# Optimization experiments

Measured on AMD Instinct MI355X. Metric: run time of the kernel, lower is better.

The kernel has to match this reference:

```python
import jax, jax.numpy as jnp
import numpy as np

EPS = 1e-6

def setup_inputs() -> dict:
    key = jax.random.key(0)
    k1, k2, k3 = jax.random.split(key, 3)
    B, N, F, OUT = 16, 1024, 64, 128
    x = jax.random.normal(k1, (B, N, F), dtype=jnp.float32)
    A = jax.random.uniform(k2, (B, N, N), dtype=jnp.float32)
    kernel = jax.random.normal(k3, (3 * F, OUT), dtype=jnp.float32) * 0.05
    bias = jnp.zeros((OUT,), dtype=jnp.float32)
    return {"x": x, "A": A, "kernel": kernel, "bias": bias}


def reference(x, A, kernel, bias):
    # x: [B,N,F], A: [B,N,N]
    n = A.shape[-1]
    eye = jnp.eye(n, dtype=A.dtype)
    Az = A * (1.0 - eye)          # zero out diagonal (A -= diag(diag_part(A)))
    A_hat = Az + eye              # add self-loops
    deg = A_hat.sum(axis=2)       # [B,N]
    inv_asym = 1.0 / (EPS + deg)                 # D^{-1}
    s = 1.0 / (EPS + jnp.sqrt(deg))              # D^{-1/2}
    # Three message-passing variants; apply diagonal scalings as broadcasts
    o1 = jnp.matmul(Az, x)                                   # A x
    o2 = inv_asym[:, :, None] * jnp.matmul(A_hat, x)         # D^{-1} A_hat x
    o3 = s[:, :, None] * jnp.matmul(A_hat, s[:, :, None] * x)  # D^{-1/2} A_hat D^{-1/2} x
    out = jnp.concatenate([o1, o2, o3], axis=-1)             # [B,N,3F]
    out = jnp.matmul(out, kernel) + bias                     # [B,N,OUT]
    return jax.nn.relu(out)
```

## Files before the change

kernel.cpp:

```cpp
#include <hip/hip_runtime.h>
#include <hip/hip_bf16.h>
#include <cstdint>

#define NN    1024
#define FF    64
#define OUTF  128
#define KCAT  192
#define EPSV  1e-6f

typedef __attribute__((ext_vector_type(4))) float  f32x4;
typedef __attribute__((ext_vector_type(8))) __bf16 bf16x8;
typedef __attribute__((ext_vector_type(4))) __bf16 bf16x4;

#define MFMA16(a, b, c) __builtin_amdgcn_mfma_f32_16x16x32_bf16(a, b, c, 0, 0, 0)
#define GLOAD_LDS16(g, l)                                          \
    __builtin_amdgcn_global_load_lds(                              \
        (const __attribute__((address_space(1))) void*)(g),        \
        (__attribute__((address_space(3))) void*)(l), 16, 0, 0)

__global__ __launch_bounds__(256) void k_deg_cvt(const float* __restrict__ A,
                                                 float* __restrict__ d1,
                                                 float* __restrict__ sArr,
                                                 __bf16* __restrict__ Az) {
    int wave = threadIdx.x >> 6;
    int lane = threadIdx.x & 63;
    int row  = blockIdx.x * 4 + wave;
    int i    = row & (NN - 1);
    const f32x4* rp = (const f32x4*)(A + (size_t)row * NN);
    __bf16* op = Az + (size_t)row * NN;
    float sum = 0.f;
#pragma unroll
    for (int t = 0; t < 4; ++t) {
        f32x4 v = rp[t * 64 + lane];
        int base = (t * 64 + lane) * 4;
#pragma unroll
        for (int q = 0; q < 4; ++q)
            if (base + q == i) v[q] = 0.f;
        sum += v[0] + v[1] + v[2] + v[3];
        bf16x4 o;
#pragma unroll
        for (int q = 0; q < 4; ++q) o[q] = (__bf16)v[q];
        *(bf16x4*)(op + base) = o;
    }
#pragma unroll
    for (int off = 32; off; off >>= 1) sum += __shfl_xor(sum, off);
    if (lane == 0) {
        float deg = 1.0f + sum;
        d1[row]   = 1.0f / (EPSV + deg);
        sArr[row] = 1.0f / (EPSV + sqrtf(deg));
    }
}

__global__ __launch_bounds__(256) void k_prep(const float* __restrict__ x,
                                              const float* __restrict__ sArr,
                                              const float* __restrict__ kern,
                                              __bf16* __restrict__ xT,
                                              __bf16* __restrict__ sxT,
                                              __bf16* __restrict__ KT) {
    __shared__ float tile[64][65];
    int bid = blockIdx.x;
    int b   = bid >> 4;
    int k0  = (bid & 15) * 64;
    const float* xp = x + ((size_t)b * NN + k0) * FF;
    for (int i = threadIdx.x; i < 64 * 64; i += 256) {
        int r = i >> 6, c = i & 63;
        tile[r][c] = xp[r * FF + c];
    }
    __syncthreads();
    for (int i = threadIdx.x; i < 64 * 64; i += 256) {
        int c = i >> 6, kk = i & 63;
        float v  = tile[kk][c];
        float sv = v * sArr[b * NN + k0 + kk];
        size_t o = ((size_t)b * FF + c) * NN + k0 + kk;
        xT[o]  = (__bf16)v;
        sxT[o] = (__bf16)sv;
    }
    if (threadIdx.x < 96) {
        int idx = bid * 96 + threadIdx.x;
        int c = idx / KCAT;
        int k = idx - c * KCAT;
        KT[idx] = (__bf16)kern[k * OUTF + c];
    }
}

__global__ __launch_bounds__(512, 4) void k_main(const __bf16* __restrict__ Az,
                                                 const float* __restrict__ x,
                                                 const float* __restrict__ bias,
                                                 const float* __restrict__ d1g,
                                                 const float* __restrict__ sg,
                                                 const __bf16* __restrict__ xT,
                                                 const __bf16* __restrict__ sxT,
                                                 const __bf16* __restrict__ KT,
                                                 float* __restrict__ out) {
    __shared__ __align__(16) char smem[65536];

    const int tid  = threadIdx.x;
    const int w    = tid >> 6;
    const int lane = tid & 63;
    const int l15  = lane & 15;
    const int h8   = (lane >> 4) * 8;

    const int work = (blockIdx.x & 7) * 64 + (blockIdx.x >> 3);
    const int b    = work >> 5;
    const int row0 = (work & 31) * 32;

    {
        const __bf16* AzB = Az + (size_t)(b * NN + row0) * NN;
        int rgl  = (tid >> 6) & 1;
        int rowL = rgl * 16 + (tid & 15);
        int colB = ((tid >> 7) * 32) + (((tid >> 4) & 3) * 8);
        const __bf16* src = AzB + (size_t)rowL * NN + colB;
        char* ldsb = smem + ((tid >> 6) << 10);
#pragma unroll
        for (int c = 0; c < 8; ++c)
            GLOAD_LDS16(src + c * 128, ldsb + c * 8192);
    }

    const int h  = w >> 2;
    const int cw = w & 3;

    const __bf16* xP = xT  + ((size_t)(b * FF + cw * 16 + l15)) * NN + h * 512 + h8;
    const __bf16* sP = sxT + ((size_t)(b * FF + cw * 16 + l15)) * NN + h * 512 + h8;
    const char* ldsA = smem + h * 32768 + lane * 16;

    asm volatile("s_waitcnt vmcnt(0)" ::: "memory");
    __syncthreads();

    f32x4 P0 = {}, P1 = {}, Q0 = {}, Q1 = {};
#pragma unroll
    for (int tt = 0; tt < 16; ++tt) {
        bf16x8 a0 = *(const bf16x8*)(ldsA + tt * 2048);
        bf16x8 a1 = *(const bf16x8*)(ldsA + tt * 2048 + 1024);
        bf16x8 xf = *(const bf16x8*)(xP + tt * 32);
        bf16x8 sf = *(const bf16x8*)(sP + tt * 32);
        P0 = MFMA16(a0, xf, P0);
        P1 = MFMA16(a1, xf, P1);
        Q0 = MFMA16(a0, sf, Q0);
        Q1 = MFMA16(a1, sf, Q1);
    }

    __syncthreads();
    f32x4* sp = (f32x4*)(smem + 32768 + cw * 4096);
    if (h == 1) {
        sp[lane]       = P0;
        sp[lane + 64]  = P1;
        sp[lane + 128] = Q0;
        sp[lane + 192] = Q1;
    }
    __syncthreads();
    __bf16 (*os)[208] = (__bf16(*)[208])smem;
    if (h == 0) {
        P0 += sp[lane];  P1 += sp[lane + 64];
        Q0 += sp[lane + 128];  Q1 += sp[lane + 192];
#pragma unroll
        for (int rg = 0; rg < 2; ++rg) {
            f32x4 Pv = rg ? P1 : P0;
            f32x4 Qv = rg ? Q1 : Q0;
#pragma unroll
            for (int j = 0; j < 4; ++j) {
                int rr   = rg * 16 + (lane >> 4) * 4 + j;
                int grow = b * NN + row0 + rr;
                float dv = d1g[grow];
                float sv = sg[grow];
                int cc   = cw * 16 + l15;
                float xv = x[(size_t)grow * FF + cc];
                os[rr][cc]        = (__bf16)Pv[j];
                os[rr][64 + cc]   = (__bf16)(dv * (Pv[j] + xv));
                os[rr][128 + cc]  = (__bf16)(sv * (Qv[j] + sv * xv));
            }
        }
    }
    __syncthreads();

    const int rge = w >> 2;
    const int cg2 = w & 3;
    f32x4 e0 = {}, e1 = {};
#pragma unroll
    for (int ks = 0; ks < 6; ++ks) {
        bf16x8 of = *(const bf16x8*)&os[rge * 16 + l15][ks * 32 + h8];
        bf16x8 k0 = *(const bf16x8*)&KT[(size_t)(cg2 * 32 + l15) * KCAT + ks * 32 + h8];
        bf16x8 k1 = *(const bf16x8*)&KT[(size_t)(cg2 * 32 + 16 + l15) * KCAT + ks * 32 + h8];
        e0 = MFMA16(of, k0, e0);
        e1 = MFMA16(of, k1, e1);
    }
#pragma unroll
    for (int g = 0; g < 2; ++g) {
        f32x4 ev = g ? e1 : e0;
        int col  = cg2 * 32 + g * 16 + l15;
        float bv = bias[col];
#pragma unroll
        for (int j = 0; j < 4; ++j) {
            int rr  = rge * 16 + (lane >> 4) * 4 + j;
            float v = ev[j] + bv;
            out[((size_t)(b * NN + row0 + rr)) * OUTF + col] = v > 0.f ? v : 0.f;
        }
    }
}

extern "C" void kernel_launch(void* const* d_in, const int* in_sizes, int n_in,
                              void* d_out, int out_size, void* d_ws, size_t ws_size,
                              hipStream_t stream) {
    const float* x    = (const float*)d_in[0];
    const float* A    = (const float*)d_in[1];
    const float* kern = (const float*)d_in[2];
    const float* bias = (const float*)d_in[3];
    float* out = (float*)d_out;

    char* ws = (char*)d_ws;
    __bf16* Az  = (__bf16*)(ws);
    float*  d1  = (float*)(ws + 33554432);
    float*  s   = (float*)(ws + 33554432 + 65536);
    __bf16* xT  = (__bf16*)(ws + 33554432 + 131072);
    __bf16* sxT = (__bf16*)(ws + 33554432 + 131072 + 2097152);
    __bf16* KT  = (__bf16*)(ws + 33554432 + 131072 + 2 * 2097152);
    (void)ws_size; (void)in_sizes; (void)n_in; (void)out_size;

    k_deg_cvt<<<dim3(4096), dim3(256), 0, stream>>>(A, d1, s, Az);
    k_prep<<<dim3(256), dim3(256), 0, stream>>>(x, s, kern, xT, sxT, KT);
    k_main<<<dim3(512), dim3(512), 0, stream>>>(Az, x, bias, d1, s, xT, sxT, KT, out);
}
```

Baseline: 138.0 us.

## Split Az LDS wait into two halves and vectorize output stores via transposed MFMA

The Az tile loads are reordered so the chunks needed for the first half of the K loop arrive first. The kernel waits with vmcnt(4) and a barrier, computes the first 8 k-steps, then waits for the rest, which overlaps compute with the remaining loads. The second GEMM swaps its MFMA operands so each lane holds four consecutive output columns. That allows 16-byte bias loads and float4 stores instead of scalar strided stores. The split wait depends on the vmcnt ordering matching the load order.

```diff
diff --git a/kernel.cpp b/kernel.cpp
--- a/kernel.cpp
+++ b/kernel.cpp
@@ -106,14 +106,16 @@
 
     {
         const __bf16* AzB = Az + (size_t)(b * NN + row0) * NN;
-        int rgl  = (tid >> 6) & 1;
-        int rowL = rgl * 16 + (tid & 15);
+        int rowL = ((tid >> 6) & 1) * 16 + (tid & 15);
         int colB = ((tid >> 7) * 32) + (((tid >> 4) & 3) * 8);
         const __bf16* src = AzB + (size_t)rowL * NN + colB;
         char* ldsb = smem + ((tid >> 6) << 10);
-#pragma unroll
-        for (int c = 0; c < 8; ++c)
+        const int corder[8] = {0, 1, 4, 5, 2, 3, 6, 7};
+#pragma unroll
+        for (int q = 0; q < 8; ++q) {
+            int c = corder[q];
             GLOAD_LDS16(src + c * 128, ldsb + c * 8192);
+        }
     }
 
     const int h  = w >> 2;
@@ -123,21 +125,30 @@
     const __bf16* sP = sxT + ((size_t)(b * FF + cw * 16 + l15)) * NN + h * 512 + h8;
     const char* ldsA = smem + h * 32768 + lane * 16;
 
+    f32x4 P0 = {}, P1 = {}, Q0 = {}, Q1 = {};
+
+#define KSTEP(tt)                                                  \
+    {                                                              \
+        bf16x8 a0 = *(const bf16x8*)(ldsA + (tt) * 2048);          \
+        bf16x8 a1 = *(const bf16x8*)(ldsA + (tt) * 2048 + 1024);   \
+        bf16x8 xf = *(const bf16x8*)(xP + (tt) * 32);              \
+        bf16x8 sf = *(const bf16x8*)(sP + (tt) * 32);              \
+        P0 = MFMA16(a0, xf, P0);                                   \
+        P1 = MFMA16(a1, xf, P1);                                   \
+        Q0 = MFMA16(a0, sf, Q0);                                   \
+        Q1 = MFMA16(a1, sf, Q1);                                   \
+    }
+
+    asm volatile("s_waitcnt vmcnt(4)" ::: "memory");
+    __builtin_amdgcn_s_barrier();
+#pragma unroll
+    for (int tt = 0; tt < 8; ++tt) KSTEP(tt)
+
     asm volatile("s_waitcnt vmcnt(0)" ::: "memory");
-    __syncthreads();
-
-    f32x4 P0 = {}, P1 = {}, Q0 = {}, Q1 = {};
-#pragma unroll
-    for (int tt = 0; tt < 16; ++tt) {
-        bf16x8 a0 = *(const bf16x8*)(ldsA + tt * 2048);
-        bf16x8 a1 = *(const bf16x8*)(ldsA + tt * 2048 + 1024);
-        bf16x8 xf = *(const bf16x8*)(xP + tt * 32);
-        bf16x8 sf = *(const bf16x8*)(sP + tt * 32);
-        P0 = MFMA16(a0, xf, P0);
-        P1 = MFMA16(a1, xf, P1);
-        Q0 = MFMA16(a0, sf, Q0);
-        Q1 = MFMA16(a1, sf, Q1);
-    }
+    __builtin_amdgcn_s_barrier();
+#pragma unroll
+    for (int tt = 8; tt < 16; ++tt) KSTEP(tt)
+#undef KSTEP
 
     __syncthreads();
     f32x4* sp = (f32x4*)(smem + 32768 + cw * 4096);
@@ -180,19 +191,23 @@
         bf16x8 of = *(const bf16x8*)&os[rge * 16 + l15][ks * 32 + h8];
         bf16x8 k0 = *(const bf16x8*)&KT[(size_t)(cg2 * 32 + l15) * KCAT + ks * 32 + h8];
         bf16x8 k1 = *(const bf16x8*)&KT[(size_t)(cg2 * 32 + 16 + l15) * KCAT + ks * 32 + h8];
-        e0 = MFMA16(of, k0, e0);
-        e1 = MFMA16(of, k1, e1);
-    }
-#pragma unroll
-    for (int g = 0; g < 2; ++g) {
-        f32x4 ev = g ? e1 : e0;
-        int col  = cg2 * 32 + g * 16 + l15;
-        float bv = bias[col];
-#pragma unroll
-        for (int j = 0; j < 4; ++j) {
-            int rr  = rge * 16 + (lane >> 4) * 4 + j;
-            float v = ev[j] + bv;
-            out[((size_t)(b * NN + row0 + rr)) * OUTF + col] = v > 0.f ? v : 0.f;
+        e0 = MFMA16(k0, of, e0);
+        e1 = MFMA16(k1, of, e1);
+    }
+    {
+        const size_t orow = (size_t)(b * NN + row0 + rge * 16 + l15) * OUTF;
+#pragma unroll
+        for (int g = 0; g < 2; ++g) {
+            f32x4 ev = g ? e1 : e0;
+            int col0 = cg2 * 32 + g * 16 + (lane >> 4) * 4;
+            f32x4 bv = *(const f32x4*)&bias[col0];
+            f32x4 r;
+#pragma unroll
+            for (int j = 0; j < 4; ++j) {
+                float v = ev[j] + bv[j];
+                r[j] = v > 0.f ? v : 0.f;
+            }
+            *(f32x4*)&out[orow + col0] = r;
         }
     }
 }
```

Measured after the change: 138.4 us. About the same (+0.3%).

## Retile main GCN kernel to 16-row blocks without split-K reduction

Applied to the files above, without the earlier changes.

The fused kernel now gives each 256-thread block 16 rows of A instead of 32. Each wave walks the full 1024-wide K range for its 16 feature columns, so the LDS split-K reduction between half-blocks and its extra barriers go away. The final projection MFMA swaps its operands so each lane holds four consecutive output columns, which allows vectorized bias loads and float4 stores. The trade-off is twice as many blocks, each re-reading the full xT/sxT slices, which doubles that operand traffic through the cache. The explicit vmcnt wait before the barrier was also removed.

```diff
diff --git a/kernel.cpp b/kernel.cpp
--- a/kernel.cpp
+++ b/kernel.cpp
@@ -83,7 +83,7 @@
     }
 }
 
-__global__ __launch_bounds__(512, 4) void k_main(const __bf16* __restrict__ Az,
+__global__ __launch_bounds__(256, 4) void k_main(const __bf16* __restrict__ Az,
                                                  const float* __restrict__ x,
                                                  const float* __restrict__ bias,
                                                  const float* __restrict__ d1g,
@@ -92,107 +92,84 @@
                                                  const __bf16* __restrict__ sxT,
                                                  const __bf16* __restrict__ KT,
                                                  float* __restrict__ out) {
-    __shared__ __align__(16) char smem[65536];
+    __shared__ __align__(16) char smem[32768];
 
     const int tid  = threadIdx.x;
-    const int w    = tid >> 6;
+    const int w4   = tid >> 6;
     const int lane = tid & 63;
     const int l15  = lane & 15;
-    const int h8   = (lane >> 4) * 8;
+    const int hi   = lane >> 4;
+    const int h8   = hi * 8;
 
-    const int work = (blockIdx.x & 7) * 64 + (blockIdx.x >> 3);
-    const int b    = work >> 5;
-    const int row0 = (work & 31) * 32;
+    const int idx  = (blockIdx.x & 7) * 128 + (blockIdx.x >> 3);
+    const int b    = idx >> 6;
+    const int row0 = (idx & 63) * 16;
 
     {
-        const __bf16* AzB = Az + (size_t)(b * NN + row0) * NN;
-        int rgl  = (tid >> 6) & 1;
-        int rowL = rgl * 16 + (tid & 15);
-        int colB = ((tid >> 7) * 32) + (((tid >> 4) & 3) * 8);
-        const __bf16* src = AzB + (size_t)rowL * NN + colB;
-        char* ldsb = smem + ((tid >> 6) << 10);
+        const __bf16* AzB = Az + (size_t)(b * NN + row0 + l15) * NN + h8;
 #pragma unroll
-        for (int c = 0; c < 8; ++c)
-            GLOAD_LDS16(src + c * 128, ldsb + c * 8192);
+        for (int c = 0; c < 8; ++c) {
+            int t = c * 4 + w4;
+            GLOAD_LDS16(AzB + t * 32, smem + t * 1024);
+        }
     }
 
-    const int h  = w >> 2;
-    const int cw = w & 3;
+    const __bf16* xPb = xT  + ((size_t)(b * FF + w4 * 16 + l15)) * NN + h8;
+    const __bf16* sPb = sxT + ((size_t)(b * FF + w4 * 16 + l15)) * NN + h8;
+    const char* ldsA = smem + lane * 16;
 
-    const __bf16* xP = xT  + ((size_t)(b * FF + cw * 16 + l15)) * NN + h * 512 + h8;
-    const __bf16* sP = sxT + ((size_t)(b * FF + cw * 16 + l15)) * NN + h * 512 + h8;
-    const char* ldsA = smem + h * 32768 + lane * 16;
-
-    asm volatile("s_waitcnt vmcnt(0)" ::: "memory");
     __syncthreads();
 
-    f32x4 P0 = {}, P1 = {}, Q0 = {}, Q1 = {};
+    f32x4 P = {}, Q = {};
 #pragma unroll
-    for (int tt = 0; tt < 16; ++tt) {
-        bf16x8 a0 = *(const bf16x8*)(ldsA + tt * 2048);
-        bf16x8 a1 = *(const bf16x8*)(ldsA + tt * 2048 + 1024);
-        bf16x8 xf = *(const bf16x8*)(xP + tt * 32);
-        bf16x8 sf = *(const bf16x8*)(sP + tt * 32);
-        P0 = MFMA16(a0, xf, P0);
-        P1 = MFMA16(a1, xf, P1);
-        Q0 = MFMA16(a0, sf, Q0);
-        Q1 = MFMA16(a1, sf, Q1);
+    for (int t = 0; t < 32; ++t) {
+        bf16x8 a  = *(const bf16x8*)(ldsA + t * 1024);
+        bf16x8 xf = *(const bf16x8*)(xPb + t * 32);
+        bf16x8 sf = *(const bf16x8*)(sPb + t * 32);
+        P = MFMA16(a, xf, P);
+        Q = MFMA16(a, sf, Q);
     }
 
     __syncthreads();
-    f32x4* sp = (f32x4*)(smem + 32768 + cw * 4096);
-    if (h == 1) {
-        sp[lane]       = P0;
-        sp[lane + 64]  = P1;
-        sp[lane + 128] = Q0;
-        sp[lane + 192] = Q1;
-    }
-    __syncthreads();
-    __bf16 (*os)[208] = (__bf16(*)[208])smem;
-    if (h == 0) {
-        P0 += sp[lane];  P1 += sp[lane + 64];
-        Q0 += sp[lane + 128];  Q1 += sp[lane + 192];
+
+    __bf16 (*os)[216] = (__bf16(*)[216])smem;
 #pragma unroll
-        for (int rg = 0; rg < 2; ++rg) {
-            f32x4 Pv = rg ? P1 : P0;
-            f32x4 Qv = rg ? Q1 : Q0;
-#pragma unroll
-            for (int j = 0; j < 4; ++j) {
-                int rr   = rg * 16 + (lane >> 4) * 4 + j;
-                int grow = b * NN + row0 + rr;
-                float dv = d1g[grow];
-                float sv = sg[grow];
-                int cc   = cw * 16 + l15;
-                float xv = x[(size_t)grow * FF + cc];
-                os[rr][cc]        = (__bf16)Pv[j];
-                os[rr][64 + cc]   = (__bf16)(dv * (Pv[j] + xv));
-                os[rr][128 + cc]  = (__bf16)(sv * (Qv[j] + sv * xv));
-            }
-        }
+    for (int j = 0; j < 4; ++j) {
+        int rr   = hi * 4 + j;
+        int grow = b * NN + row0 + rr;
+        float dv = d1g[grow];
+        float sv = sg[grow];
+        int cc   = w4 * 16 + l15;
+        float xv = x[(size_t)grow * FF + cc];
+        os[rr][cc]       = (__bf16)P[j];
+        os[rr][64 + cc]  = (__bf16)(dv * (P[j] + xv));
+        os[rr][128 + cc] = (__bf16)(sv * (Q[j] + sv * xv));
     }
     __syncthreads();
 
-    const int rge = w >> 2;
-    const int cg2 = w & 3;
     f32x4 e0 = {}, e1 = {};
 #pragma unroll
     for (int ks = 0; ks < 6; ++ks) {
-        bf16x8 of = *(const bf16x8*)&os[rge * 16 + l15][ks * 32 + h8];
-        bf16x8 k0 = *(const bf16x8*)&KT[(size_t)(cg2 * 32 + l15) * KCAT + ks * 32 + h8];
-        bf16x8 k1 = *(const bf16x8*)&KT[(size_t)(cg2 * 32 + 16 + l15) * KCAT + ks * 32 + h8];
-        e0 = MFMA16(of, k0, e0);
-        e1 = MFMA16(of, k1, e1);
+        bf16x8 of = *(const bf16x8*)&os[l15][ks * 32 + h8];
+        bf16x8 k0 = *(const bf16x8*)&KT[(size_t)(w4 * 32 + l15) * KCAT + ks * 32 + h8];
+        bf16x8 k1 = *(const bf16x8*)&KT[(size_t)(w4 * 32 + 16 + l15) * KCAT + ks * 32 + h8];
+        e0 = MFMA16(k0, of, e0);
+        e1 = MFMA16(k1, of, e1);
     }
+    {
+        const size_t orow = (size_t)(b * NN + row0 + l15) * OUTF;
 #pragma unroll
-    for (int g = 0; g < 2; ++g) {
-        f32x4 ev = g ? e1 : e0;
-        int col  = cg2 * 32 + g * 16 + l15;
-        float bv = bias[col];
+        for (int g = 0; g < 2; ++g) {
+            f32x4 ev = g ? e1 : e0;
+            int col0 = w4 * 32 + g * 16 + hi * 4;
+            f32x4 bv = *(const f32x4*)&bias[col0];
+            f32x4 rv;
 #pragma unroll
-        for (int j = 0; j < 4; ++j) {
-            int rr  = rge * 16 + (lane >> 4) * 4 + j;
-            float v = ev[j] + bv;
-            out[((size_t)(b * NN + row0 + rr)) * OUTF + col] = v > 0.f ? v : 0.f;
+            for (int j = 0; j < 4; ++j) {
+                float v = ev[j] + bv[j];
+                rv[j] = v > 0.f ? v : 0.f;
+            }
+            *(f32x4*)&out[orow + col0] = rv;
         }
     }
 }
@@ -217,5 +194,5 @@
 
     k_deg_cvt<<<dim3(4096), dim3(256), 0, stream>>>(A, d1, s, Az);
     k_prep<<<dim3(256), dim3(256), 0, stream>>>(x, s, kern, xT, sxT, KT);
-    k_main<<<dim3(512), dim3(512), 0, stream>>>(Az, x, bias, d1, s, xT, sxT, KT, out);
+    k_main<<<dim3(1024), dim3(256), 0, stream>>>(Az, x, bias, d1, s, xT, sxT, KT, out);
 }
```

Result: slower. 150.7 us (+9.2%).
